# Performance work log

Measured on AMD Instinct MI355X. Metric: run time of the kernel, lower is better.

The kernel has to match this reference:

```python
import jax, jax.numpy as jnp
import numpy as np

B, S, H, NH = 2, 2048, 2048, 16
HD = H // NH
SCALE = 1.0 / np.sqrt(HD).astype(np.float32)


def setup_inputs() -> dict:
    key = jax.random.key(0)
    ks = jax.random.split(key, 11)
    std = 1.0 / np.sqrt(H)
    inp = {
        'query': jax.random.normal(ks[0], (B, S, H), dtype=jnp.float32),
        'key': jax.random.normal(ks[1], (B, S, H), dtype=jnp.float32),
        'value': jax.random.normal(ks[2], (B, S, H), dtype=jnp.float32),
        'Wq': jax.random.normal(ks[3], (H, H), dtype=jnp.float32) * std,
        'bq': jax.random.normal(ks[4], (H,), dtype=jnp.float32) * std,
        'Wk': jax.random.normal(ks[5], (H, H), dtype=jnp.float32) * std,
        'bk': jax.random.normal(ks[6], (H,), dtype=jnp.float32) * std,
        'Wv': jax.random.normal(ks[7], (H, H), dtype=jnp.float32) * std,
        'bv': jax.random.normal(ks[8], (H,), dtype=jnp.float32) * std,
        'Wo': jax.random.normal(ks[9], (H, H), dtype=jnp.float32) * std,
        'bo': jax.random.normal(ks[10], (H,), dtype=jnp.float32) * std,
    }
    return inp


def reference(query, key, value, Wq, bq, Wk, bk, Wv, bv, Wo, bo):
    # Linear projections (torch Linear: x @ W.T + b)
    q = query @ Wq.T + bq
    k = key @ Wk.T + bk
    v = value @ Wv.T + bv
    # [B, NH, S, HD]
    q = q.reshape(B, S, NH, HD).transpose(0, 2, 1, 3)
    k = k.reshape(B, S, NH, HD).transpose(0, 2, 1, 3)
    v = v.reshape(B, S, NH, HD).transpose(0, 2, 1, 3)
    scores = jnp.einsum('bhqd,bhkd->bhqk', q, k) * SCALE
    attn = jax.nn.softmax(scores, axis=-1)  # dropout p=0 (eval)
    ctx = jnp.einsum('bhqk,bhkd->bhqd', attn, v)
    ctx = ctx.transpose(0, 2, 1, 3).reshape(B, S, H)
    out = ctx @ Wo.T + bo
    return out
```

## Files before the change

### kernel.cpp

```cpp
#include <hip/hip_runtime.h>


typedef __bf16 bf16_t;
typedef __bf16 bf16x8 __attribute__((ext_vector_type(8)));
typedef float  f32x4  __attribute__((ext_vector_type(4)));

#define DEVI __device__ __forceinline__

DEVI void async_copy16(const void* gsrc, void* ldst) {
  __builtin_amdgcn_global_load_lds(
      (const __attribute__((address_space(1))) unsigned int*)gsrc,
      (__attribute__((address_space(3))) unsigned int*)ldst, 16, 0, 0);
}

constexpr int Bc = 2, Sc = 2048, Hc = 2048, NHc = 16, HDc = 128;
constexpr float SCALE_LOG2E = 0.12751744550358464f;
constexpr int PSTR = 72;

DEVI void cast_body(const float* __restrict__ in, bf16_t* __restrict__ out) {
  int i = (blockIdx.x * 256 + threadIdx.x) * 8;
  float4 f0 = *(const float4*)(in + i);
  float4 f1 = *(const float4*)(in + i + 4);
  union { bf16_t h[8]; uint4 u; } o;
  o.h[0] = (bf16_t)f0.x; o.h[1] = (bf16_t)f0.y;
  o.h[2] = (bf16_t)f0.z; o.h[3] = (bf16_t)f0.w;
  o.h[4] = (bf16_t)f1.x; o.h[5] = (bf16_t)f1.y;
  o.h[6] = (bf16_t)f1.z; o.h[7] = (bf16_t)f1.w;
  *(uint4*)(out + i) = o.u;
}

__global__ void cast3(const float* __restrict__ a, const float* __restrict__ b,
                      const float* __restrict__ c, bf16_t* __restrict__ oa,
                      bf16_t* __restrict__ ob, bf16_t* __restrict__ oc) {
  const float* src = blockIdx.y == 0 ? a : blockIdx.y == 1 ? b : c;
  bf16_t* dst = blockIdx.y == 0 ? oa : blockIdx.y == 1 ? ob : oc;
  cast_body(src, dst);
}

__global__ void cast4(const float* __restrict__ a, const float* __restrict__ b,
                      const float* __restrict__ c, const float* __restrict__ d,
                      bf16_t* __restrict__ oa, bf16_t* __restrict__ ob,
                      bf16_t* __restrict__ oc, bf16_t* __restrict__ od) {
  const float* src = blockIdx.y == 0 ? a : blockIdx.y == 1 ? b
                   : blockIdx.y == 2 ? c : d;
  bf16_t* dst = blockIdx.y == 0 ? oa : blockIdx.y == 1 ? ob
              : blockIdx.y == 2 ? oc : od;
  cast_body(src, dst);
}

template <int M, int N, int K>
DEVI void gemm_body(const bf16_t* __restrict__ A, const bf16_t* __restrict__ Bw,
                    const float* __restrict__ bias, void* __restrict__ Cout,
                    float scale, int out_mode) {
  constexpr int BM = 256, BN = 128, BK = 64;
  constexpr int NT = K / BK;
  constexpr int SLOT = (BM + BN) * BK;
  __shared__ __align__(16) bf16_t lds[3 * SLOT];

  const int tid = threadIdx.x;
  const int lane = tid & 63;
  const int wave = tid >> 6;
  const int bm = blockIdx.x & (M / BM - 1);
  const int bn = blockIdx.x / (M / BM);
  const int wm = wave >> 1, wn = wave & 1;
  const int quad = lane >> 4, l15 = lane & 15;

  const bf16_t* Abase = A + (size_t)bm * BM * K;
  const bf16_t* Bbase = Bw + (size_t)bn * BN * K;
  const bf16_t* asrc0; const bf16_t* asrc1; const bf16_t* asrc2; const bf16_t* asrc3;
  const bf16_t* bsrc0; const bf16_t* bsrc1;
  int aoff0, aoff1, aoff2, aoff3, boff0, boff1;
  {
    int i0 = wave * 4;
    int r0 = i0 * 8 + (lane >> 3);       aoff0 = i0 * 512;
    int r1 = (i0 + 1) * 8 + (lane >> 3); aoff1 = (i0 + 1) * 512;
    int r2 = (i0 + 2) * 8 + (lane >> 3); aoff2 = (i0 + 2) * 512;
    int r3 = (i0 + 3) * 8 + (lane >> 3); aoff3 = (i0 + 3) * 512;
    asrc0 = Abase + (size_t)r0 * K + (((lane & 7) ^ (r0 & 7)) * 8);
    asrc1 = Abase + (size_t)r1 * K + (((lane & 7) ^ (r1 & 7)) * 8);
    asrc2 = Abase + (size_t)r2 * K + (((lane & 7) ^ (r2 & 7)) * 8);
    asrc3 = Abase + (size_t)r3 * K + (((lane & 7) ^ (r3 & 7)) * 8);
    int j0 = wave * 2;
    int s0 = j0 * 8 + (lane >> 3);       boff0 = BM * BK + j0 * 512;
    int s1 = (j0 + 1) * 8 + (lane >> 3); boff1 = BM * BK + (j0 + 1) * 512;
    bsrc0 = Bbase + (size_t)s0 * K + (((lane & 7) ^ (s0 & 7)) * 8);
    bsrc1 = Bbase + (size_t)s1 * K + (((lane & 7) ^ (s1 & 7)) * 8);
  }

  f32x4 zero4 = {0.f, 0.f, 0.f, 0.f};
  f32x4 acc[4][4];
#pragma unroll
  for (int i = 0; i < 4; ++i)
#pragma unroll
    for (int j = 0; j < 4; ++j) acc[i][j] = zero4;

  int arow[4], brow[4];
#pragma unroll
  for (int t = 0; t < 4; ++t) {
    arow[t] = wm * 64 + t * 16 + l15;
    brow[t] = wn * 64 + t * 16 + l15;
  }

  auto stage_half0 = [&](int kt) {
    bf16_t* slot = lds + (kt % 3) * SLOT;
    int k0 = kt * BK;
    async_copy16(asrc0 + k0, slot + aoff0);
    async_copy16(asrc1 + k0, slot + aoff1);
    async_copy16(bsrc0 + k0, slot + boff0);
  };
  auto stage_half1 = [&](int kt) {
    bf16_t* slot = lds + (kt % 3) * SLOT;
    int k0 = kt * BK;
    async_copy16(asrc2 + k0, slot + aoff2);
    async_copy16(asrc3 + k0, slot + aoff3);
    async_copy16(bsrc1 + k0, slot + boff1);
  };

  stage_half0(0); stage_half1(0);
  stage_half0(1); stage_half1(1);

  for (int kt = 0; kt < NT; ++kt) {
    if (kt + 1 < NT) {
      asm volatile("s_waitcnt vmcnt(6)" ::: "memory");
    } else {
      asm volatile("s_waitcnt vmcnt(0)" ::: "memory");
    }
    __builtin_amdgcn_s_barrier();
    asm volatile("" ::: "memory");

    const bf16_t* As = lds + (kt % 3) * SLOT;
    const bf16_t* Bs = As + BM * BK;
    const bool do_stage = (kt + 2 < NT);

#pragma unroll
    for (int ks = 0; ks < 2; ++ks) {
      if (do_stage) {
        if (ks == 0) stage_half0(kt + 2);
        else         stage_half1(kt + 2);
      }
      bf16x8 af[4], bfv[4];
#pragma unroll
      for (int mt = 0; mt < 4; ++mt)
        af[mt] = *(const bf16x8*)(As + arow[mt] * 64 +
                                  (((ks * 4 + quad) ^ (arow[mt] & 7)) * 8));
#pragma unroll
      for (int nt = 0; nt < 4; ++nt)
        bfv[nt] = *(const bf16x8*)(Bs + brow[nt] * 64 +
                                   (((ks * 4 + quad) ^ (brow[nt] & 7)) * 8));
      __builtin_amdgcn_s_setprio(1);
#pragma unroll
      for (int mt = 0; mt < 4; ++mt)
#pragma unroll
        for (int nt = 0; nt < 4; ++nt)
          acc[mt][nt] = __builtin_amdgcn_mfma_f32_16x16x32_bf16(
              af[mt], bfv[nt], acc[mt][nt], 0, 0, 0);
      __builtin_amdgcn_s_setprio(0);
    }
    __syncthreads();
  }

  float bv[4];
#pragma unroll
  for (int nt = 0; nt < 4; ++nt) bv[nt] = bias[bn * BN + brow[nt]];

#pragma unroll
  for (int mt = 0; mt < 4; ++mt) {
    const int rbase = bm * BM + wm * 64 + mt * 16 + quad * 4;
#pragma unroll
    for (int nt = 0; nt < 4; ++nt) {
      const int col = bn * BN + brow[nt];
      if (out_mode == 0) {
        bf16_t* C = (bf16_t*)Cout;
#pragma unroll
        for (int r = 0; r < 4; ++r)
          C[(size_t)(rbase + r) * N + col] = (bf16_t)((acc[mt][nt][r] + bv[nt]) * scale);
      } else if (out_mode == 2) {
        float* C = (float*)Cout;
#pragma unroll
        for (int r = 0; r < 4; ++r)
          C[(size_t)(rbase + r) * N + col] = acc[mt][nt][r] + bv[nt];
      } else {
        bf16_t* C = (bf16_t*)Cout;
        const int bb = rbase >> 11;
        const int s0 = rbase & (Sc - 1);
        const int h = col >> 7, d = col & (HDc - 1);
        union { bf16_t h4[4]; uint2 u; } o;
#pragma unroll
        for (int r = 0; r < 4; ++r) o.h4[r] = (bf16_t)(acc[mt][nt][r] + bv[nt]);
        *(uint2*)(C + (((size_t)(bb * NHc + h) * HDc + d) * Sc + s0)) = o.u;
      }
    }
  }
}

__global__ __launch_bounds__(512, 2) void qkv_proj(
    const bf16_t* __restrict__ Xq, const bf16_t* __restrict__ Xk,
    const bf16_t* __restrict__ Xv, const bf16_t* __restrict__ Wq,
    const bf16_t* __restrict__ Wk, const bf16_t* __restrict__ Wv,
    const float* __restrict__ bq, const float* __restrict__ bk,
    const float* __restrict__ bv, bf16_t* __restrict__ q,
    bf16_t* __restrict__ k, bf16_t* __restrict__ vt) {
  const int p = blockIdx.y;
  const bf16_t* A = p == 0 ? Xq : p == 1 ? Xk : Xv;
  const bf16_t* W = p == 0 ? Wq : p == 1 ? Wk : Wv;
  const float* bi = p == 0 ? bq : p == 1 ? bk : bv;
  void* out = p == 0 ? (void*)q : p == 1 ? (void*)k : (void*)vt;
  gemm_body<4096, 2048, 2048>(A, W, bi, out, p == 0 ? SCALE_LOG2E : 1.0f,
                              p == 2 ? 1 : 0);
}

__global__ __launch_bounds__(512, 2) void o_proj(
    const bf16_t* __restrict__ A, const bf16_t* __restrict__ W,
    const float* __restrict__ bi, float* __restrict__ out) {
  gemm_body<4096, 2048, 2048>(A, W, bi, out, 1.0f, 2);
}

__global__ __launch_bounds__(256, 2) void flash_attn(const bf16_t* __restrict__ Q,
                                                     const bf16_t* __restrict__ Kg,
                                                     const bf16_t* __restrict__ Vt,
                                                     bf16_t* __restrict__ ctx) {
  __shared__ __align__(16) bf16_t smem[2 * 64 * 128 + 128 * 64 + 4 * 32 * PSTR];
  bf16_t* Ks0 = smem;
  bf16_t* Ks1 = smem + 8192;
  bf16_t* Vs = smem + 16384;
  bf16_t* Ps = smem + 24576;

  const int tid = threadIdx.x, lane = tid & 63, wave = tid >> 6;
  const int quad = lane >> 4, l15 = lane & 15;
  const int bid = blockIdx.x;
  const int qt = bid & 15, h = (bid >> 4) & 15, b = bid >> 8;

  bf16_t* Pw = Ps + wave * (32 * PSTR);

  bf16x8 qf[2][4];
#pragma unroll
  for (int mt = 0; mt < 2; ++mt) {
    int grow = b * Sc + qt * 128 + wave * 32 + mt * 16 + l15;
    const bf16_t* qp = Q + (size_t)grow * Hc + h * HDc;
#pragma unroll
    for (int kc = 0; kc < 4; ++kc) qf[mt][kc] = *(const bf16x8*)(qp + kc * 32 + quad * 8);
  }

  f32x4 zero4 = {0.f, 0.f, 0.f, 0.f};
  f32x4 o[2][8];
#pragma unroll
  for (int mt = 0; mt < 2; ++mt)
#pragma unroll
    for (int dt = 0; dt < 8; ++dt) o[mt][dt] = zero4;
  float mrow[2][4], lpart[2][4];
#pragma unroll
  for (int mt = 0; mt < 2; ++mt)
#pragma unroll
    for (int r = 0; r < 4; ++r) { mrow[mt][r] = -1e30f; lpart[mt][r] = 0.f; }

  int kr_[4], kc_[4], vr_[4], vc_[4];
#pragma unroll
  for (int i = 0; i < 4; ++i) {
    int s = wave * 4 + i;
    kr_[i] = s * 4 + quad;        kc_[i] = l15 ^ (kr_[i] & 7);
    vr_[i] = s * 8 + (lane >> 3); vc_[i] = (lane & 7) ^ (vr_[i] & 7);
  }
  const bf16_t* Kbase = Kg + (size_t)b * Sc * Hc + h * HDc;
  const bf16_t* Vbase = Vt + (size_t)(b * NHc + h) * HDc * Sc;

  auto stageK = [&](int kb, bf16_t* dst) {
#pragma unroll
    for (int i = 0; i < 4; ++i)
      async_copy16(Kbase + (size_t)(kb * 64 + kr_[i]) * Hc + kc_[i] * 8,
                   dst + (wave * 4 + i) * 512);
  };
  auto stageV = [&](int kb) {
#pragma unroll
    for (int i = 0; i < 4; ++i)
      async_copy16(Vbase + (size_t)vr_[i] * Sc + kb * 64 + vc_[i] * 8,
                   Vs + (wave * 4 + i) * 512);
  };

  stageK(0, Ks0);
  stageV(0);
  stageK(1, Ks1);

  for (int kb = 0; kb < 32; ++kb) {
    bf16_t* Kcur = (kb & 1) ? Ks1 : Ks0;

    if (kb + 1 < 32) asm volatile("s_waitcnt vmcnt(8)" ::: "memory");
    else             asm volatile("s_waitcnt vmcnt(4)" ::: "memory");
    __builtin_amdgcn_s_barrier();
    asm volatile("" ::: "memory");

    f32x4 sf[2][4];
#pragma unroll
    for (int mt = 0; mt < 2; ++mt)
#pragma unroll
      for (int nt = 0; nt < 4; ++nt) sf[mt][nt] = zero4;
#pragma unroll
    for (int kc = 0; kc < 4; ++kc)
#pragma unroll
      for (int nt = 0; nt < 4; ++nt) {
        int kr = nt * 16 + l15;
        bf16x8 kf = *(const bf16x8*)(Kcur + kr * 128 + (((kc * 4 + quad) ^ (kr & 7)) * 8));
        sf[0][nt] = __builtin_amdgcn_mfma_f32_16x16x32_bf16(qf[0][kc], kf, sf[0][nt], 0, 0, 0);
        sf[1][nt] = __builtin_amdgcn_mfma_f32_16x16x32_bf16(qf[1][kc], kf, sf[1][nt], 0, 0, 0);
      }

    float lmx[2][4];
    bool need = false;
#pragma unroll
    for (int mt = 0; mt < 2; ++mt)
#pragma unroll
      for (int r = 0; r < 4; ++r) {
        float m0 = fmaxf(fmaxf(sf[mt][0][r], sf[mt][1][r]),
                         fmaxf(sf[mt][2][r], sf[mt][3][r]));
        lmx[mt][r] = m0;
        need = need || (m0 > mrow[mt][r] + 8.0f);
      }
    if (__any(need)) {
#pragma unroll
      for (int mt = 0; mt < 2; ++mt)
#pragma unroll
        for (int r = 0; r < 4; ++r) {
          float mx = lmx[mt][r];
#pragma unroll
          for (int off = 1; off < 16; off <<= 1) mx = fmaxf(mx, __shfl_xor(mx, off));
          float mnew = fmaxf(mrow[mt][r], mx);
          float alpha = __builtin_amdgcn_exp2f(mrow[mt][r] - mnew);
          mrow[mt][r] = mnew;
          lpart[mt][r] *= alpha;
#pragma unroll
          for (int dt = 0; dt < 8; ++dt) o[mt][dt][r] *= alpha;
        }
    }
#pragma unroll
    for (int mt = 0; mt < 2; ++mt)
#pragma unroll
      for (int r = 0; r < 4; ++r) {
        float p0 = __builtin_amdgcn_exp2f(sf[mt][0][r] - mrow[mt][r]);
        float p1 = __builtin_amdgcn_exp2f(sf[mt][1][r] - mrow[mt][r]);
        float p2 = __builtin_amdgcn_exp2f(sf[mt][2][r] - mrow[mt][r]);
        float p3 = __builtin_amdgcn_exp2f(sf[mt][3][r] - mrow[mt][r]);
        sf[mt][0][r] = p0; sf[mt][1][r] = p1;
        sf[mt][2][r] = p2; sf[mt][3][r] = p3;
        lpart[mt][r] += (p0 + p1) + (p2 + p3);
      }

#pragma unroll
    for (int mt = 0; mt < 2; ++mt)
#pragma unroll
      for (int nt = 0; nt < 4; ++nt)
#pragma unroll
        for (int r = 0; r < 4; ++r)
          Pw[(mt * 16 + quad * 4 + r) * PSTR + nt * 16 + l15] = (bf16_t)sf[mt][nt][r];

    bf16x8 pf[2][2];
#pragma unroll
    for (int mt = 0; mt < 2; ++mt) {
      const bf16_t* pr = Pw + (mt * 16 + l15) * PSTR;
#pragma unroll
      for (int kc = 0; kc < 2; ++kc)
        pf[mt][kc] = *(const bf16x8*)(pr + kc * 32 + quad * 8);
    }

    if (kb + 1 < 32) asm volatile("s_waitcnt vmcnt(4)" ::: "memory");
    else             asm volatile("s_waitcnt vmcnt(0)" ::: "memory");
    __builtin_amdgcn_s_barrier();
    asm volatile("" ::: "memory");

#pragma unroll
    for (int kc = 0; kc < 2; ++kc)
#pragma unroll
      for (int dt = 0; dt < 8; ++dt) {
        int vr = dt * 16 + l15;
        bf16x8 vf = *(const bf16x8*)(Vs + vr * 64 + (((kc * 4 + quad) ^ (vr & 7)) * 8));
        o[0][dt] = __builtin_amdgcn_mfma_f32_16x16x32_bf16(pf[0][kc], vf, o[0][dt], 0, 0, 0);
        o[1][dt] = __builtin_amdgcn_mfma_f32_16x16x32_bf16(pf[1][kc], vf, o[1][dt], 0, 0, 0);
      }

    __builtin_amdgcn_s_barrier();
    asm volatile("" ::: "memory");
    if (kb + 1 < 32) stageV(kb + 1);
    if (kb + 2 < 32) stageK(kb + 2, Kcur);
  }

  __syncthreads();
  bf16_t* Ow = smem + wave * 4096;
#pragma unroll
  for (int mt = 0; mt < 2; ++mt) {
    float rinv[4];
#pragma unroll
    for (int r = 0; r < 4; ++r) {
      float l = lpart[mt][r];
#pragma unroll
      for (int off = 1; off < 16; off <<= 1) l += __shfl_xor(l, off);
      rinv[r] = 1.f / l;
    }
#pragma unroll
    for (int dt = 0; dt < 8; ++dt)
#pragma unroll
      for (int r = 0; r < 4; ++r)
        Ow[(mt * 16 + quad * 4 + r) * 128 + dt * 16 + l15] = (bf16_t)(o[mt][dt][r] * rinv[r]);
  }
#pragma unroll
  for (int r = 0; r < 32; ++r) {
    unsigned v = *(const unsigned*)(Ow + r * 128 + lane * 2);
    int grow = b * Sc + qt * 128 + wave * 32 + r;
    *(unsigned*)(ctx + (size_t)grow * Hc + h * HDc + lane * 2) = v;
  }
}

extern "C" void kernel_launch(void* const* d_in, const int* in_sizes, int n_in,
                              void* d_out, int out_size, void* d_ws, size_t ws_size,
                              hipStream_t stream) {
  const float* query = (const float*)d_in[0];
  const float* key_i = (const float*)d_in[1];
  const float* value = (const float*)d_in[2];
  const float* Wq = (const float*)d_in[3];
  const float* bq = (const float*)d_in[4];
  const float* Wk = (const float*)d_in[5];
  const float* bk = (const float*)d_in[6];
  const float* Wv = (const float*)d_in[7];
  const float* bv = (const float*)d_in[8];
  const float* Wo = (const float*)d_in[9];
  const float* bo = (const float*)d_in[10];

  const size_t XE = (size_t)Bc * Sc * Hc;
  const size_t WE = (size_t)Hc * Hc;
  const size_t need = 6 * XE * 2 + 4 * WE * 2;
  if (ws_size < need) return;

  char* ws = (char*)d_ws;
  size_t off = 0;
  auto alloc = [&](size_t bytes) {
    char* p = ws + off;
    off += (bytes + 255) & ~(size_t)255;
    return p;
  };
  bf16_t* Xq = (bf16_t*)alloc(XE * 2);
  bf16_t* Xk = (bf16_t*)alloc(XE * 2);
  bf16_t* Xv = (bf16_t*)alloc(XE * 2);
  bf16_t* Wqb = (bf16_t*)alloc(WE * 2);
  bf16_t* Wkb = (bf16_t*)alloc(WE * 2);
  bf16_t* Wvb = (bf16_t*)alloc(WE * 2);
  bf16_t* Wob = (bf16_t*)alloc(WE * 2);
  bf16_t* qb = (bf16_t*)alloc(XE * 2);
  bf16_t* kb = (bf16_t*)alloc(XE * 2);
  bf16_t* vtb = (bf16_t*)alloc(XE * 2);
  bf16_t* ctxb = Xq;

  cast3<<<dim3((unsigned)(XE / 2048), 3), 256, 0, stream>>>(query, key_i, value, Xq, Xk, Xv);
  cast4<<<dim3((unsigned)(WE / 2048), 4), 256, 0, stream>>>(Wq, Wk, Wv, Wo, Wqb, Wkb, Wvb, Wob);

  qkv_proj<<<dim3(256, 3), 512, 0, stream>>>(Xq, Xk, Xv, Wqb, Wkb, Wvb,
                                             bq, bk, bv, qb, kb, vtb);

  flash_attn<<<512, 256, 0, stream>>>(qb, kb, vtb, ctxb);

  o_proj<<<256, 512, 0, stream>>>(ctxb, Wob, bo, (float*)d_out);
}
```

Baseline: 418.6 us.

## Swap MFMA operands to keep P in registers, removing LDS round-trip

The attention kernel now computes S^T by swapping the MFMA operands, so each lane holds four keys for one query row. The softmax probabilities can then be packed directly into bf16x8 operands for the PV MFMA without going through shared memory. To make the register layout of P match the V operand, the V-projection epilogue writes Vt with a permuted sequence order. The P staging buffer is removed, which shrinks LDS so launch bounds can allow three blocks per CU, and row max and sum reductions drop to two cross-lane shuffles.

```diff
diff --git a/kernel.cpp b/kernel.cpp
--- a/kernel.cpp
+++ b/kernel.cpp
@@ -15,7 +15,6 @@
 
 constexpr int Bc = 2, Sc = 2048, Hc = 2048, NHc = 16, HDc = 128;
 constexpr float SCALE_LOG2E = 0.12751744550358464f;
-constexpr int PSTR = 72;
 
 DEVI void cast_body(const float* __restrict__ in, bf16_t* __restrict__ out) {
   int i = (blockIdx.x * 256 + threadIdx.x) * 8;
@@ -183,11 +182,13 @@
         bf16_t* C = (bf16_t*)Cout;
         const int bb = rbase >> 11;
         const int s0 = rbase & (Sc - 1);
+        const int sp = (s0 & ~63) | (s0 & 32) | ((s0 & 12) << 1) |
+                       ((s0 & 16) >> 2) | (s0 & 3);
         const int h = col >> 7, d = col & (HDc - 1);
         union { bf16_t h4[4]; uint2 u; } o;
 #pragma unroll
         for (int r = 0; r < 4; ++r) o.h4[r] = (bf16_t)(acc[mt][nt][r] + bv[nt]);
-        *(uint2*)(C + (((size_t)(bb * NHc + h) * HDc + d) * Sc + s0)) = o.u;
+        *(uint2*)(C + (((size_t)(bb * NHc + h) * HDc + d) * Sc + sp)) = o.u;
       }
     }
   }
@@ -215,23 +216,20 @@
   gemm_body<4096, 2048, 2048>(A, W, bi, out, 1.0f, 2);
 }
 
-__global__ __launch_bounds__(256, 2) void flash_attn(const bf16_t* __restrict__ Q,
+__global__ __launch_bounds__(256, 3) void flash_attn(const bf16_t* __restrict__ Q,
                                                      const bf16_t* __restrict__ Kg,
                                                      const bf16_t* __restrict__ Vt,
                                                      bf16_t* __restrict__ ctx) {
-  __shared__ __align__(16) bf16_t smem[2 * 64 * 128 + 128 * 64 + 4 * 32 * PSTR];
+  __shared__ __align__(16) bf16_t smem[3 * 8192];
   bf16_t* Ks0 = smem;
   bf16_t* Ks1 = smem + 8192;
   bf16_t* Vs = smem + 16384;
-  bf16_t* Ps = smem + 24576;
 
   const int tid = threadIdx.x, lane = tid & 63, wave = tid >> 6;
   const int quad = lane >> 4, l15 = lane & 15;
   const int bid = blockIdx.x;
   const int qt = bid & 15, h = (bid >> 4) & 15, b = bid >> 8;
 
-  bf16_t* Pw = Ps + wave * (32 * PSTR);
-
   bf16x8 qf[2][4];
 #pragma unroll
   for (int mt = 0; mt < 2; ++mt) {
@@ -247,11 +245,8 @@
   for (int mt = 0; mt < 2; ++mt)
 #pragma unroll
     for (int dt = 0; dt < 8; ++dt) o[mt][dt] = zero4;
-  float mrow[2][4], lpart[2][4];
-#pragma unroll
-  for (int mt = 0; mt < 2; ++mt)
-#pragma unroll
-    for (int r = 0; r < 4; ++r) { mrow[mt][r] = -1e30f; lpart[mt][r] = 0.f; }
+  float mrow[2] = {-1e30f, -1e30f};
+  float lpart[2] = {0.f, 0.f};
 
   int kr_[4], kc_[4], vr_[4], vc_[4];
 #pragma unroll
@@ -299,65 +294,52 @@
       for (int nt = 0; nt < 4; ++nt) {
         int kr = nt * 16 + l15;
         bf16x8 kf = *(const bf16x8*)(Kcur + kr * 128 + (((kc * 4 + quad) ^ (kr & 7)) * 8));
-        sf[0][nt] = __builtin_amdgcn_mfma_f32_16x16x32_bf16(qf[0][kc], kf, sf[0][nt], 0, 0, 0);
-        sf[1][nt] = __builtin_amdgcn_mfma_f32_16x16x32_bf16(qf[1][kc], kf, sf[1][nt], 0, 0, 0);
-      }
-
-    float lmx[2][4];
-    bool need = false;
-#pragma unroll
-    for (int mt = 0; mt < 2; ++mt)
-#pragma unroll
-      for (int r = 0; r < 4; ++r) {
-        float m0 = fmaxf(fmaxf(sf[mt][0][r], sf[mt][1][r]),
-                         fmaxf(sf[mt][2][r], sf[mt][3][r]));
-        lmx[mt][r] = m0;
-        need = need || (m0 > mrow[mt][r] + 8.0f);
-      }
+        sf[0][nt] = __builtin_amdgcn_mfma_f32_16x16x32_bf16(kf, qf[0][kc], sf[0][nt], 0, 0, 0);
+        sf[1][nt] = __builtin_amdgcn_mfma_f32_16x16x32_bf16(kf, qf[1][kc], sf[1][nt], 0, 0, 0);
+      }
+
+    float lm[2];
+#pragma unroll
+    for (int mt = 0; mt < 2; ++mt) {
+      float m4[4];
+#pragma unroll
+      for (int nt = 0; nt < 4; ++nt)
+        m4[nt] = fmaxf(fmaxf(sf[mt][nt][0], sf[mt][nt][1]),
+                       fmaxf(sf[mt][nt][2], sf[mt][nt][3]));
+      lm[mt] = fmaxf(fmaxf(m4[0], m4[1]), fmaxf(m4[2], m4[3]));
+    }
+    bool need = (lm[0] > mrow[0] + 8.0f) || (lm[1] > mrow[1] + 8.0f);
     if (__any(need)) {
 #pragma unroll
-      for (int mt = 0; mt < 2; ++mt)
-#pragma unroll
-        for (int r = 0; r < 4; ++r) {
-          float mx = lmx[mt][r];
-#pragma unroll
-          for (int off = 1; off < 16; off <<= 1) mx = fmaxf(mx, __shfl_xor(mx, off));
-          float mnew = fmaxf(mrow[mt][r], mx);
-          float alpha = __builtin_amdgcn_exp2f(mrow[mt][r] - mnew);
-          mrow[mt][r] = mnew;
-          lpart[mt][r] *= alpha;
-#pragma unroll
-          for (int dt = 0; dt < 8; ++dt) o[mt][dt][r] *= alpha;
-        }
-    }
-#pragma unroll
-    for (int mt = 0; mt < 2; ++mt)
-#pragma unroll
-      for (int r = 0; r < 4; ++r) {
-        float p0 = __builtin_amdgcn_exp2f(sf[mt][0][r] - mrow[mt][r]);
-        float p1 = __builtin_amdgcn_exp2f(sf[mt][1][r] - mrow[mt][r]);
-        float p2 = __builtin_amdgcn_exp2f(sf[mt][2][r] - mrow[mt][r]);
-        float p3 = __builtin_amdgcn_exp2f(sf[mt][3][r] - mrow[mt][r]);
-        sf[mt][0][r] = p0; sf[mt][1][r] = p1;
-        sf[mt][2][r] = p2; sf[mt][3][r] = p3;
-        lpart[mt][r] += (p0 + p1) + (p2 + p3);
-      }
-
-#pragma unroll
-    for (int mt = 0; mt < 2; ++mt)
-#pragma unroll
-      for (int nt = 0; nt < 4; ++nt)
-#pragma unroll
-        for (int r = 0; r < 4; ++r)
-          Pw[(mt * 16 + quad * 4 + r) * PSTR + nt * 16 + l15] = (bf16_t)sf[mt][nt][r];
-
-    bf16x8 pf[2][2];
+      for (int mt = 0; mt < 2; ++mt) {
+        float mx = lm[mt];
+        mx = fmaxf(mx, __shfl_xor(mx, 16));
+        mx = fmaxf(mx, __shfl_xor(mx, 32));
+        float mnew = fmaxf(mrow[mt], mx);
+        float alpha = __builtin_amdgcn_exp2f(mrow[mt] - mnew);
+        mrow[mt] = mnew;
+        lpart[mt] *= alpha;
+#pragma unroll
+        for (int dt = 0; dt < 8; ++dt) o[mt][dt] *= alpha;
+      }
+    }
+
+    union { bf16_t hh[8]; bf16x8 v; } pb8[2][2];
 #pragma unroll
     for (int mt = 0; mt < 2; ++mt) {
-      const bf16_t* pr = Pw + (mt * 16 + l15) * PSTR;
-#pragma unroll
-      for (int kc = 0; kc < 2; ++kc)
-        pf[mt][kc] = *(const bf16x8*)(pr + kc * 32 + quad * 8);
+#pragma unroll
+      for (int nt = 0; nt < 4; ++nt) {
+        float p0 = __builtin_amdgcn_exp2f(sf[mt][nt][0] - mrow[mt]);
+        float p1 = __builtin_amdgcn_exp2f(sf[mt][nt][1] - mrow[mt]);
+        float p2 = __builtin_amdgcn_exp2f(sf[mt][nt][2] - mrow[mt]);
+        float p3 = __builtin_amdgcn_exp2f(sf[mt][nt][3] - mrow[mt]);
+        lpart[mt] += (p0 + p1) + (p2 + p3);
+        const int pr = nt >> 1, bo = (nt & 1) * 4;
+        pb8[mt][pr].hh[bo + 0] = (bf16_t)p0;
+        pb8[mt][pr].hh[bo + 1] = (bf16_t)p1;
+        pb8[mt][pr].hh[bo + 2] = (bf16_t)p2;
+        pb8[mt][pr].hh[bo + 3] = (bf16_t)p3;
+      }
     }
 
     if (kb + 1 < 32) asm volatile("s_waitcnt vmcnt(4)" ::: "memory");
@@ -366,13 +348,13 @@
     asm volatile("" ::: "memory");
 
 #pragma unroll
-    for (int kc = 0; kc < 2; ++kc)
+    for (int pr = 0; pr < 2; ++pr)
 #pragma unroll
       for (int dt = 0; dt < 8; ++dt) {
         int vr = dt * 16 + l15;
-        bf16x8 vf = *(const bf16x8*)(Vs + vr * 64 + (((kc * 4 + quad) ^ (vr & 7)) * 8));
-        o[0][dt] = __builtin_amdgcn_mfma_f32_16x16x32_bf16(pf[0][kc], vf, o[0][dt], 0, 0, 0);
-        o[1][dt] = __builtin_amdgcn_mfma_f32_16x16x32_bf16(pf[1][kc], vf, o[1][dt], 0, 0, 0);
+        bf16x8 vf = *(const bf16x8*)(Vs + vr * 64 + (((pr * 4 + quad) ^ (vr & 7)) * 8));
+        o[0][dt] = __builtin_amdgcn_mfma_f32_16x16x32_bf16(vf, pb8[0][pr].v, o[0][dt], 0, 0, 0);
+        o[1][dt] = __builtin_amdgcn_mfma_f32_16x16x32_bf16(vf, pb8[1][pr].v, o[1][dt], 0, 0, 0);
       }
 
     __builtin_amdgcn_s_barrier();
@@ -382,26 +364,24 @@
   }
 
   __syncthreads();
-  bf16_t* Ow = smem + wave * 4096;
+  bf16_t* Ow = smem + wave * (32 * 136);
 #pragma unroll
   for (int mt = 0; mt < 2; ++mt) {
-    float rinv[4];
-#pragma unroll
-    for (int r = 0; r < 4; ++r) {
-      float l = lpart[mt][r];
-#pragma unroll
-      for (int off = 1; off < 16; off <<= 1) l += __shfl_xor(l, off);
-      rinv[r] = 1.f / l;
-    }
-#pragma unroll
-    for (int dt = 0; dt < 8; ++dt)
-#pragma unroll
-      for (int r = 0; r < 4; ++r)
-        Ow[(mt * 16 + quad * 4 + r) * 128 + dt * 16 + l15] = (bf16_t)(o[mt][dt][r] * rinv[r]);
+    float l = lpart[mt];
+    l += __shfl_xor(l, 16);
+    l += __shfl_xor(l, 32);
+    float rinv = 1.f / l;
+#pragma unroll
+    for (int dt = 0; dt < 8; ++dt) {
+      union { bf16_t h4[4]; uint2 u; } t;
+#pragma unroll
+      for (int r = 0; r < 4; ++r) t.h4[r] = (bf16_t)(o[mt][dt][r] * rinv);
+      *(uint2*)(Ow + (mt * 16 + l15) * 136 + dt * 16 + quad * 4) = t.u;
+    }
   }
 #pragma unroll
   for (int r = 0; r < 32; ++r) {
-    unsigned v = *(const unsigned*)(Ow + r * 128 + lane * 2);
+    unsigned v = *(const unsigned*)(Ow + r * 136 + lane * 2);
     int grow = b * Sc + qt * 128 + wave * 32 + r;
     *(unsigned*)(ctx + (size_t)grow * Hc + h * HDc + lane * 2) = v;
   }
```

After: 462.4 us. 1.1x slower.

## Split flash attention work across eight waves with one 16-row tile each

Applied to the files above, without the earlier changes.

The flash attention block goes from 4 waves handling 32 query rows each to 8 waves handling 16 rows each, keeping the 128-row tile per block. Per-wave accumulators, Q fragments and P scratch are halved, and each wave issues half as many async K/V copies, so the vmcnt thresholds are halved to match. This lowers register pressure and raises the number of waves available to hide latency. In exchange, each K/V fragment loaded from LDS now feeds one MFMA instead of two, doubling LDS read traffic per unit of compute, and barriers now synchronise more waves.

```diff
diff --git a/kernel.cpp b/kernel.cpp
--- a/kernel.cpp
+++ b/kernel.cpp
@@ -215,11 +215,11 @@
   gemm_body<4096, 2048, 2048>(A, W, bi, out, 1.0f, 2);
 }
 
-__global__ __launch_bounds__(256, 2) void flash_attn(const bf16_t* __restrict__ Q,
+__global__ __launch_bounds__(512, 2) void flash_attn(const bf16_t* __restrict__ Q,
                                                      const bf16_t* __restrict__ Kg,
                                                      const bf16_t* __restrict__ Vt,
                                                      bf16_t* __restrict__ ctx) {
-  __shared__ __align__(16) bf16_t smem[2 * 64 * 128 + 128 * 64 + 4 * 32 * PSTR];
+  __shared__ __align__(16) bf16_t smem[2 * 64 * 128 + 128 * 64 + 8 * 16 * PSTR];
   bf16_t* Ks0 = smem;
   bf16_t* Ks1 = smem + 8192;
   bf16_t* Vs = smem + 16384;
@@ -230,33 +230,28 @@
   const int bid = blockIdx.x;
   const int qt = bid & 15, h = (bid >> 4) & 15, b = bid >> 8;
 
-  bf16_t* Pw = Ps + wave * (32 * PSTR);
-
-  bf16x8 qf[2][4];
-#pragma unroll
-  for (int mt = 0; mt < 2; ++mt) {
-    int grow = b * Sc + qt * 128 + wave * 32 + mt * 16 + l15;
+  bf16_t* Pw = Ps + wave * (16 * PSTR);
+
+  bf16x8 qf[4];
+  {
+    int grow = b * Sc + qt * 128 + wave * 16 + l15;
     const bf16_t* qp = Q + (size_t)grow * Hc + h * HDc;
 #pragma unroll
-    for (int kc = 0; kc < 4; ++kc) qf[mt][kc] = *(const bf16x8*)(qp + kc * 32 + quad * 8);
+    for (int kc = 0; kc < 4; ++kc) qf[kc] = *(const bf16x8*)(qp + kc * 32 + quad * 8);
   }
 
   f32x4 zero4 = {0.f, 0.f, 0.f, 0.f};
-  f32x4 o[2][8];
-#pragma unroll
-  for (int mt = 0; mt < 2; ++mt)
-#pragma unroll
-    for (int dt = 0; dt < 8; ++dt) o[mt][dt] = zero4;
-  float mrow[2][4], lpart[2][4];
-#pragma unroll
-  for (int mt = 0; mt < 2; ++mt)
-#pragma unroll
-    for (int r = 0; r < 4; ++r) { mrow[mt][r] = -1e30f; lpart[mt][r] = 0.f; }
-
-  int kr_[4], kc_[4], vr_[4], vc_[4];
-#pragma unroll
-  for (int i = 0; i < 4; ++i) {
-    int s = wave * 4 + i;
+  f32x4 o[8];
+#pragma unroll
+  for (int dt = 0; dt < 8; ++dt) o[dt] = zero4;
+  float mrow[4], lpart[4];
+#pragma unroll
+  for (int r = 0; r < 4; ++r) { mrow[r] = -1e30f; lpart[r] = 0.f; }
+
+  int kr_[2], kc_[2], vr_[2], vc_[2];
+#pragma unroll
+  for (int i = 0; i < 2; ++i) {
+    int s = wave * 2 + i;
     kr_[i] = s * 4 + quad;        kc_[i] = l15 ^ (kr_[i] & 7);
     vr_[i] = s * 8 + (lane >> 3); vc_[i] = (lane & 7) ^ (vr_[i] & 7);
   }
@@ -265,15 +260,15 @@
 
   auto stageK = [&](int kb, bf16_t* dst) {
 #pragma unroll
-    for (int i = 0; i < 4; ++i)
+    for (int i = 0; i < 2; ++i)
       async_copy16(Kbase + (size_t)(kb * 64 + kr_[i]) * Hc + kc_[i] * 8,
-                   dst + (wave * 4 + i) * 512);
+                   dst + (wave * 2 + i) * 512);
   };
   auto stageV = [&](int kb) {
 #pragma unroll
-    for (int i = 0; i < 4; ++i)
+    for (int i = 0; i < 2; ++i)
       async_copy16(Vbase + (size_t)vr_[i] * Sc + kb * 64 + vc_[i] * 8,
-                   Vs + (wave * 4 + i) * 512);
+                   Vs + (wave * 2 + i) * 512);
   };
 
   stageK(0, Ks0);
@@ -283,84 +278,70 @@
   for (int kb = 0; kb < 32; ++kb) {
     bf16_t* Kcur = (kb & 1) ? Ks1 : Ks0;
 
-    if (kb + 1 < 32) asm volatile("s_waitcnt vmcnt(8)" ::: "memory");
-    else             asm volatile("s_waitcnt vmcnt(4)" ::: "memory");
+    if (kb + 1 < 32) asm volatile("s_waitcnt vmcnt(4)" ::: "memory");
+    else             asm volatile("s_waitcnt vmcnt(2)" ::: "memory");
     __builtin_amdgcn_s_barrier();
     asm volatile("" ::: "memory");
 
-    f32x4 sf[2][4];
-#pragma unroll
-    for (int mt = 0; mt < 2; ++mt)
-#pragma unroll
-      for (int nt = 0; nt < 4; ++nt) sf[mt][nt] = zero4;
+    f32x4 sf[4];
+#pragma unroll
+    for (int nt = 0; nt < 4; ++nt) sf[nt] = zero4;
 #pragma unroll
     for (int kc = 0; kc < 4; ++kc)
 #pragma unroll
       for (int nt = 0; nt < 4; ++nt) {
         int kr = nt * 16 + l15;
         bf16x8 kf = *(const bf16x8*)(Kcur + kr * 128 + (((kc * 4 + quad) ^ (kr & 7)) * 8));
-        sf[0][nt] = __builtin_amdgcn_mfma_f32_16x16x32_bf16(qf[0][kc], kf, sf[0][nt], 0, 0, 0);
-        sf[1][nt] = __builtin_amdgcn_mfma_f32_16x16x32_bf16(qf[1][kc], kf, sf[1][nt], 0, 0, 0);
+        sf[nt] = __builtin_amdgcn_mfma_f32_16x16x32_bf16(qf[kc], kf, sf[nt], 0, 0, 0);
       }
 
-    float lmx[2][4];
+    float lmx[4];
     bool need = false;
 #pragma unroll
-    for (int mt = 0; mt < 2; ++mt)
+    for (int r = 0; r < 4; ++r) {
+      float m0 = fmaxf(fmaxf(sf[0][r], sf[1][r]), fmaxf(sf[2][r], sf[3][r]));
+      lmx[r] = m0;
+      need = need || (m0 > mrow[r] + 8.0f);
+    }
+    if (__any(need)) {
 #pragma unroll
       for (int r = 0; r < 4; ++r) {
-        float m0 = fmaxf(fmaxf(sf[mt][0][r], sf[mt][1][r]),
-                         fmaxf(sf[mt][2][r], sf[mt][3][r]));
-        lmx[mt][r] = m0;
-        need = need || (m0 > mrow[mt][r] + 8.0f);
+        float mx = lmx[r];
+#pragma unroll
+        for (int off = 1; off < 16; off <<= 1) mx = fmaxf(mx, __shfl_xor(mx, off));
+        float mnew = fmaxf(mrow[r], mx);
+        float alpha = __builtin_amdgcn_exp2f(mrow[r] - mnew);
+        mrow[r] = mnew;
+        lpart[r] *= alpha;
+#pragma unroll
+        for (int dt = 0; dt < 8; ++dt) o[dt][r] *= alpha;
       }
-    if (__any(need)) {
-#pragma unroll
-      for (int mt = 0; mt < 2; ++mt)
-#pragma unroll
-        for (int r = 0; r < 4; ++r) {
-          float mx = lmx[mt][r];
-#pragma unroll
-          for (int off = 1; off < 16; off <<= 1) mx = fmaxf(mx, __shfl_xor(mx, off));
-          float mnew = fmaxf(mrow[mt][r], mx);
-          float alpha = __builtin_amdgcn_exp2f(mrow[mt][r] - mnew);
-          mrow[mt][r] = mnew;
-          lpart[mt][r] *= alpha;
-#pragma unroll
-          for (int dt = 0; dt < 8; ++dt) o[mt][dt][r] *= alpha;
-        }
-    }
-#pragma unroll
-    for (int mt = 0; mt < 2; ++mt)
-#pragma unroll
-      for (int r = 0; r < 4; ++r) {
-        float p0 = __builtin_amdgcn_exp2f(sf[mt][0][r] - mrow[mt][r]);
-        float p1 = __builtin_amdgcn_exp2f(sf[mt][1][r] - mrow[mt][r]);
-        float p2 = __builtin_amdgcn_exp2f(sf[mt][2][r] - mrow[mt][r]);
-        float p3 = __builtin_amdgcn_exp2f(sf[mt][3][r] - mrow[mt][r]);
-        sf[mt][0][r] = p0; sf[mt][1][r] = p1;
-        sf[mt][2][r] = p2; sf[mt][3][r] = p3;
-        lpart[mt][r] += (p0 + p1) + (p2 + p3);
-      }
-
-#pragma unroll
-    for (int mt = 0; mt < 2; ++mt)
-#pragma unroll
-      for (int nt = 0; nt < 4; ++nt)
-#pragma unroll
-        for (int r = 0; r < 4; ++r)
-          Pw[(mt * 16 + quad * 4 + r) * PSTR + nt * 16 + l15] = (bf16_t)sf[mt][nt][r];
-
-    bf16x8 pf[2][2];
-#pragma unroll
-    for (int mt = 0; mt < 2; ++mt) {
-      const bf16_t* pr = Pw + (mt * 16 + l15) * PSTR;
+    }
+#pragma unroll
+    for (int r = 0; r < 4; ++r) {
+      float p0 = __builtin_amdgcn_exp2f(sf[0][r] - mrow[r]);
+      float p1 = __builtin_amdgcn_exp2f(sf[1][r] - mrow[r]);
+      float p2 = __builtin_amdgcn_exp2f(sf[2][r] - mrow[r]);
+      float p3 = __builtin_amdgcn_exp2f(sf[3][r] - mrow[r]);
+      sf[0][r] = p0; sf[1][r] = p1; sf[2][r] = p2; sf[3][r] = p3;
+      lpart[r] += (p0 + p1) + (p2 + p3);
+    }
+
+#pragma unroll
+    for (int nt = 0; nt < 4; ++nt)
+#pragma unroll
+      for (int r = 0; r < 4; ++r)
+        Pw[(quad * 4 + r) * PSTR + nt * 16 + l15] = (bf16_t)sf[nt][r];
+
+    bf16x8 pf[2];
+    {
+      const bf16_t* pr = Pw + l15 * PSTR;
 #pragma unroll
       for (int kc = 0; kc < 2; ++kc)
-        pf[mt][kc] = *(const bf16x8*)(pr + kc * 32 + quad * 8);
-    }
-
-    if (kb + 1 < 32) asm volatile("s_waitcnt vmcnt(4)" ::: "memory");
+        pf[kc] = *(const bf16x8*)(pr + kc * 32 + quad * 8);
+    }
+
+    if (kb + 1 < 32) asm volatile("s_waitcnt vmcnt(2)" ::: "memory");
     else             asm volatile("s_waitcnt vmcnt(0)" ::: "memory");
     __builtin_amdgcn_s_barrier();
     asm volatile("" ::: "memory");
@@ -371,8 +352,7 @@
       for (int dt = 0; dt < 8; ++dt) {
         int vr = dt * 16 + l15;
         bf16x8 vf = *(const bf16x8*)(Vs + vr * 64 + (((kc * 4 + quad) ^ (vr & 7)) * 8));
-        o[0][dt] = __builtin_amdgcn_mfma_f32_16x16x32_bf16(pf[0][kc], vf, o[0][dt], 0, 0, 0);
-        o[1][dt] = __builtin_amdgcn_mfma_f32_16x16x32_bf16(pf[1][kc], vf, o[1][dt], 0, 0, 0);
+        o[dt] = __builtin_amdgcn_mfma_f32_16x16x32_bf16(pf[kc], vf, o[dt], 0, 0, 0);
       }
 
     __builtin_amdgcn_s_barrier();
@@ -382,13 +362,12 @@
   }
 
   __syncthreads();
-  bf16_t* Ow = smem + wave * 4096;
-#pragma unroll
-  for (int mt = 0; mt < 2; ++mt) {
+  bf16_t* Ow = smem + wave * 2048;
+  {
     float rinv[4];
 #pragma unroll
     for (int r = 0; r < 4; ++r) {
-      float l = lpart[mt][r];
+      float l = lpart[r];
 #pragma unroll
       for (int off = 1; off < 16; off <<= 1) l += __shfl_xor(l, off);
       rinv[r] = 1.f / l;
@@ -397,12 +376,12 @@
     for (int dt = 0; dt < 8; ++dt)
 #pragma unroll
       for (int r = 0; r < 4; ++r)
-        Ow[(mt * 16 + quad * 4 + r) * 128 + dt * 16 + l15] = (bf16_t)(o[mt][dt][r] * rinv[r]);
-  }
-#pragma unroll
-  for (int r = 0; r < 32; ++r) {
+        Ow[(quad * 4 + r) * 128 + dt * 16 + l15] = (bf16_t)(o[dt][r] * rinv[r]);
+  }
+#pragma unroll
+  for (int r = 0; r < 16; ++r) {
     unsigned v = *(const unsigned*)(Ow + r * 128 + lane * 2);
-    int grow = b * Sc + qt * 128 + wave * 32 + r;
+    int grow = b * Sc + qt * 128 + wave * 16 + r;
     *(unsigned*)(ctx + (size_t)grow * Hc + h * HDc + lane * 2) = v;
   }
 }
@@ -452,7 +431,7 @@
   qkv_proj<<<dim3(256, 3), 512, 0, stream>>>(Xq, Xk, Xv, Wqb, Wkb, Wvb,
                                              bq, bk, bv, qb, kb, vtb);
 
-  flash_attn<<<512, 256, 0, stream>>>(qb, kb, vtb, ctxb);
+  flash_attn<<<512, 512, 0, stream>>>(qb, kb, vtb, ctxb);
 
   o_proj<<<256, 512, 0, stream>>>(ctxb, Wob, bo, (float*)d_out);
 }
```

New measurement: 422.1 us. Within noise of the previous version (+0.8%).
